# Kernel tuning notes

Hardware: AMD Instinct MI355X
Metric: run time of the kernel (lower is better)

Reference implementation:

```python
import jax, jax.numpy as jnp
import numpy as np

N_NODES = 100000
N_EDGES = 3200000
H, D = 3, 12  # heads, per-head dim; H*D == node_hidden_dim == 36
NEG_SLOPE = 0.2


def setup_inputs() -> dict:
    key = jax.random.key(0)
    ks = jax.random.split(key, 11)
    s = 0.1
    return {
        "node_features": jax.random.normal(ks[0], (N_NODES, 36), jnp.float32),
        "src": jax.random.randint(ks[1], (N_EDGES,), 0, N_NODES),
        "dst": jax.random.randint(ks[2], (N_EDGES,), 0, N_NODES),
        "lin0_w": jax.random.normal(ks[3], (36, 36), jnp.float32) * s,
        "lin0_b": jax.random.normal(ks[4], (36,), jnp.float32) * s,
        "fc_w": jax.random.normal(ks[5], (3, 36, 36), jnp.float32) * s,
        "attn_l": jax.random.normal(ks[6], (3, H, D), jnp.float32) * s,
        "attn_r": jax.random.normal(ks[7], (3, H, D), jnp.float32) * s,
        "gat_bias": jax.random.normal(ks[8], (3, 36), jnp.float32) * s,
        "out_w": jax.random.normal(ks[9], (36, 36), jnp.float32) * s,
        "out_b": jax.random.normal(ks[10], (36,), jnp.float32) * s,
    }


def _gat_layer(h, src, dst, fc_w, a_l, a_r, bias):
    n = h.shape[0]
    feat = (h @ fc_w).reshape(n, H, D)                      # (N,H,D)
    el = jnp.sum(feat * a_l, axis=-1)                       # (N,H)
    er = jnp.sum(feat * a_r, axis=-1)                       # (N,H)
    e = el[src] + er[dst]                                   # (E,H)
    e = jnp.where(e >= 0, e, NEG_SLOPE * e)                 # leaky_relu(0.2)
    # edge softmax over incoming edges of each dst node (numerically stable)
    m = jax.ops.segment_max(e, dst, num_segments=n)         # (N,H)
    m = jnp.where(jnp.isfinite(m), m, 0.0)                  # zero-degree guard
    ee = jnp.exp(e - m[dst])                                # (E,H)
    denom = jax.ops.segment_sum(ee, dst, num_segments=n)    # (N,H)
    alpha = ee / jnp.maximum(denom[dst], 1e-9)              # (E,H)
    msg = feat[src] * alpha[:, :, None]                     # (E,H,D)
    rst = jax.ops.segment_sum(msg, dst, num_segments=n)     # (N,H,D)
    # residual (Identity since in_feats == H*D) + bias, then ELU
    rst = rst + h.reshape(n, H, D) + bias.reshape(1, H, D)
    return jax.nn.elu(rst).reshape(n, H * D)


def reference(node_features, src, dst, lin0_w, lin0_b, fc_w, attn_l, attn_r, gat_bias, out_w, out_b):
    h = node_features @ lin0_w + lin0_b
    for l in range(3):
        h = _gat_layer(h, src, dst, fc_w[l], attn_l[l], attn_r[l], gat_bias[l])
    return h @ out_w + out_b
```

## Files before the change

### kernel.cpp

```cpp
#include <hip/hip_runtime.h>
#include <math.h>

#define HID 36
#define NH 3
#define HD 12
#define PROW 64
#define BSHIFT 13
#define NBUCK 13
#define PSHIFT 8
#define PCHUNK 2048
#define SPCAP 9216
#define CSRCAP 4096
#define NSTEP 8

typedef _Float16 f16;


__global__ void hist2_kernel(const int* __restrict__ dst, int* __restrict__ M,
                             int E, int C, int np) {
    __shared__ int h[512];
    int t = threadIdx.x;
    int c = blockIdx.x;
    for (int i = t; i < 512; i += blockDim.x) h[i] = 0;
    __syncthreads();
    int i0 = c * PCHUNK;
    int i1 = min(i0 + PCHUNK, E);
    for (int i = i0 + t; i < i1; i += blockDim.x)
        atomicAdd(&h[dst[i] >> PSHIFT], 1);
    __syncthreads();
    for (int b = t; b < np; b += blockDim.x)
        M[(size_t)b * C + c] = h[b];
}

__global__ void base_scan_kernel(const int* __restrict__ M, int* __restrict__ BaseT,
                                 int* __restrict__ T, int C, int np) {
    __shared__ int tmp[512];
    int b = blockIdx.x;
    int t = threadIdx.x;
    int carry = 0;
    for (int base = 0; base < C; base += 512) {
        int idx = base + t;
        int v = (idx < C) ? M[(size_t)b * C + idx] : 0;
        tmp[t] = v;
        __syncthreads();
        for (int ofs = 1; ofs < 512; ofs <<= 1) {
            int x = 0;
            if (t >= ofs) x = tmp[t - ofs];
            __syncthreads();
            tmp[t] += x;
            __syncthreads();
        }
        if (idx < C) BaseT[(size_t)idx * 512 + b] = carry + tmp[t] - v;
        carry += tmp[511];
        __syncthreads();
    }
    if (t == 0) T[b] = carry;
}

__global__ void scan_small_kernel(const int* __restrict__ T, int* __restrict__ poff, int np) {
    __shared__ int tmp[512];
    int t = threadIdx.x;
    int v = (t < np) ? T[t] : 0;
    tmp[t] = v;
    __syncthreads();
    for (int ofs = 1; ofs < 512; ofs <<= 1) {
        int x = 0;
        if (t >= ofs) x = tmp[t - ofs];
        __syncthreads();
        tmp[t] += x;
        __syncthreads();
    }
    int excl = tmp[t] - v;
    if (t < np) poff[t] = excl;
    if (t == np - 1) poff[np] = excl + v;
}

__global__ void part_scatter_kernel(const int* __restrict__ src, const int* __restrict__ dst,
                                    const int* __restrict__ BaseT, const int* __restrict__ poff,
                                    int* __restrict__ part, int E, int np) {
    __shared__ int h[512];
    __shared__ int base[512];
    int t = threadIdx.x;
    int c = blockIdx.x;
    for (int i = t; i < 512; i += blockDim.x) h[i] = 0;
    for (int b = t; b < np; b += blockDim.x)
        base[b] = poff[b] + BaseT[(size_t)c * 512 + b];
    __syncthreads();
    int i0 = c * PCHUNK;
    int i1 = min(i0 + PCHUNK, E);
    for (int i = i0 + t; i < i1; i += blockDim.x) {
        int d = dst[i];
        int bin = d >> PSHIFT;
        int r = atomicAdd(&h[bin], 1);
        part[base[bin] + r] = (src[i] << PSHIFT) | (d & ((1 << PSHIFT) - 1));
    }
}

__global__ void bucket_csr_kernel(const int* __restrict__ part, const int* __restrict__ T,
                                  const int* __restrict__ poff,
                                  int* __restrict__ csr, int* __restrict__ off,
                                  int n, int E) {
    __shared__ int cnt[256 * NBUCK];
    __shared__ int psum[512];
    __shared__ int smpart[SPCAP];
    int p = blockIdx.x;
    int t = threadIdx.x;
    int dbase = p << PSHIFT;
    int nd = min(256, n - dbase);
    int nc = nd * NBUCK;
    for (int i = t; i < nc; i += blockDim.x) cnt[i] = 0;
    __syncthreads();
    int cnt_p = T[p];
    int e0 = poff[p];
    const int* pp = part + e0;
    bool fits = (cnt_p <= SPCAP);
    for (int i = t; i < cnt_p; i += blockDim.x) {
        int e = pp[i];
        if (fits) smpart[i] = e;
        atomicAdd(&cnt[(e & 255) * NBUCK + ((e >> PSHIFT) >> BSHIFT)], 1);
    }
    __syncthreads();
    int sum = 0;
    if (t < nd) {
        for (int k = 0; k < NBUCK; ++k) {
            int c = cnt[t * NBUCK + k];
            cnt[t * NBUCK + k] = sum;
            sum += c;
        }
    }
    psum[t] = (t < nd) ? sum : 0;
    __syncthreads();
    for (int ofs = 1; ofs < 512; ofs <<= 1) {
        int x = 0;
        if (t >= ofs) x = psum[t - ofs];
        __syncthreads();
        psum[t] += x;
        __syncthreads();
    }
    int dexcl = (t > 0) ? psum[t - 1] : 0;
    int start = e0 + dexcl;
    if (t < nd) {
        for (int k = 0; k < NBUCK; ++k) cnt[t * NBUCK + k] += start;
        off[dbase + t] = start;
    }
    __syncthreads();
    for (int i = t; i < cnt_p; i += blockDim.x) {
        int e = fits ? smpart[i] : pp[i];
        int s = e >> PSHIFT;
        int idx = (e & 255) * NBUCK + (s >> BSHIFT);
        int pos = atomicAdd(&cnt[idx], 1);
        csr[pos] = s << 6;
    }
    if (p == 0 && t == 0) off[n] = E;
}


__device__ __forceinline__ void edge_accum(uint4 qa, uint4 qb, float ern,
                                           float& denom, float* acc) {
    union { uint4 q[2]; f16 hx[16]; } v;
    v.q[0] = qa;
    v.q[1] = qb;
    float e = (float)v.hx[12] + ern;
    e = (e >= 0.f) ? e : 0.2f * e;
    float w = __expf(e);
    denom += w;
#pragma unroll
    for (int k = 0; k < HD; ++k) acc[k] += w * (float)v.hx[k];
}

template <bool FITS>
__device__ __forceinline__ void sweep_paced(const int* __restrict__ smbuf,
                                            const int* __restrict__ csre,
                                            int j0, int deg, const f16* __restrict__ pb,
                                            float ern, float& denom, float* acc) {
    int j = j0;
#pragma unroll 1
    for (int s2 = 1; s2 <= NSTEP; ++s2) {
        int jend = j0 + ((deg * s2) >> 3);
        int c = jend - j;
        for (; c >= 4; c -= 4, j += 4) {
            int o0 = FITS ? smbuf[j]     : csre[j];
            int o1 = FITS ? smbuf[j + 1] : csre[j + 1];
            int o2 = FITS ? smbuf[j + 2] : csre[j + 2];
            int o3 = FITS ? smbuf[j + 3] : csre[j + 3];
            const uint4* r0 = (const uint4*)(pb + o0);
            const uint4* r1 = (const uint4*)(pb + o1);
            const uint4* r2 = (const uint4*)(pb + o2);
            const uint4* r3 = (const uint4*)(pb + o3);
            uint4 a0 = r0[0], b0 = r0[1];
            uint4 a1 = r1[0], b1 = r1[1];
            uint4 a2 = r2[0], b2 = r2[1];
            uint4 a3 = r3[0], b3 = r3[1];
            edge_accum(a0, b0, ern, denom, acc);
            edge_accum(a1, b1, ern, denom, acc);
            edge_accum(a2, b2, ern, denom, acc);
            edge_accum(a3, b3, ern, denom, acc);
        }
        for (; c > 0; --c, ++j) {
            int o = FITS ? smbuf[j] : csre[j];
            const uint4* r = (const uint4*)(pb + o);
            edge_accum(r[0], r[1], ern, denom, acc);
        }
    }
}

__global__ void __launch_bounds__(256, 1)
lin0tr_kernel(const float* __restrict__ x, const float* __restrict__ w0,
              const float* __restrict__ b0, const float* __restrict__ fcw,
              const float* __restrict__ al, const float* __restrict__ ar,
              float* __restrict__ h, f16* __restrict__ packed,
              float* __restrict__ er, int n) {
    __shared__ float W0[HID * HID];
    __shared__ float W1[HID * HID];
    __shared__ float Bs[HID], ALs[HID], ARs[HID];
    int t = threadIdx.x;
    for (int i = t; i < HID * HID; i += 256) { W0[i] = w0[i]; W1[i] = fcw[i]; }
    if (t < HID) { Bs[t] = b0[t]; ALs[t] = al[t]; ARs[t] = ar[t]; }
    __syncthreads();
    int node = blockIdx.x * 256 + t;
    if (node >= n) return;
    const float4* xp = (const float4*)(x + (size_t)node * HID);
    float h0[HID];
#pragma unroll
    for (int j = 0; j < HID; ++j) h0[j] = Bs[j];
#pragma unroll
    for (int kk = 0; kk < HID / 4; ++kk) {
        float4 xv = xp[kk];
        const float* w = &W0[(4 * kk) * HID];
#pragma unroll
        for (int j = 0; j < HID; ++j)
            h0[j] += xv.x * w[j] + xv.y * w[HID + j] + xv.z * w[2 * HID + j] + xv.w * w[3 * HID + j];
    }
    float* hp = h + (size_t)node * HID;
#pragma unroll
    for (int j = 0; j < HID; ++j) hp[j] = h0[j];
    float feat[HID];
#pragma unroll
    for (int j = 0; j < HID; ++j) feat[j] = 0.f;
#pragma unroll
    for (int k = 0; k < HID; ++k) {
        float hv = h0[k];
        const float* w = &W1[k * HID];
#pragma unroll
        for (int j = 0; j < HID; ++j) feat[j] += hv * w[j];
    }
    union { f16 hx[48]; uint4 q[6]; } u;
#pragma unroll
    for (int hh = 0; hh < NH; ++hh) {
        float sl = 0.f, sr = 0.f;
#pragma unroll
        for (int d = 0; d < HD; ++d) {
            sl += feat[hh * HD + d] * ALs[hh * HD + d];
            sr += feat[hh * HD + d] * ARs[hh * HD + d];
        }
#pragma unroll
        for (int d = 0; d < HD; ++d) u.hx[hh * 16 + d] = (f16)feat[hh * HD + d];
        u.hx[hh * 16 + 12] = (f16)sl;
        u.hx[hh * 16 + 13] = (f16)0.f;
        u.hx[hh * 16 + 14] = (f16)0.f;
        u.hx[hh * 16 + 15] = (f16)0.f;
        er[node * NH + hh] = sr;
    }
    uint4* prow = (uint4*)(packed + (size_t)node * PROW);
#pragma unroll
    for (int q = 0; q < 6; ++q) prow[q] = u.q[q];
}

__global__ void __launch_bounds__(192)
aggtr_kernel(const f16* __restrict__ packed_in, const float* __restrict__ er_in,
             const float* __restrict__ hcur,
             const int* __restrict__ off, const int* __restrict__ csr,
             const float* __restrict__ bias, const float* __restrict__ wnext,
             const float* __restrict__ aln, const float* __restrict__ arn,
             float* __restrict__ hnext, f16* __restrict__ packed_out,
             float* __restrict__ er_out, int n) {
    __shared__ float Wsh[HID * HID];
    __shared__ float ALs[HID], ARs[HID];
    __shared__ int smbuf[CSRCAP];
    int t = threadIdx.x;
    for (int i = t; i < HID * HID; i += 192) Wsh[i] = wnext[i];
    if (t < HID) { ALs[t] = aln[t]; ARs[t] = arn[t]; }
    int ln = t / 3, hh = t - ln * 3;
    int nb0 = blockIdx.x * 64;
    int node = nb0 + ln;
    bool active = (node < n);

    int e0 = off[nb0];
    int e1 = off[min(nb0 + 64, n)];
    int span = e1 - e0;
    bool fits = (span <= CSRCAP);
    if (fits)
        for (int i = t; i < span; i += 192) smbuf[i] = csr[e0 + i];

    int j0 = 0, deg = 0;
    float ern = 0.f;
    if (active) {
        j0 = off[node] - e0;
        deg = off[node + 1] - e0 - j0;
        ern = er_in[node * NH + hh];
    }
    const f16* pb = packed_in + hh * 16;
    const int* csre = csr + e0;
    __syncthreads();

    float denom = 0.f;
    float acc[HD];
#pragma unroll
    for (int k = 0; k < HD; ++k) acc[k] = 0.f;

    if (fits) sweep_paced<true>(smbuf, csre, j0, deg, pb, ern, denom, acc);
    else      sweep_paced<false>(smbuf, csre, j0, deg, pb, ern, denom, acc);
    __syncthreads();

    float* hsh = (float*)smbuf;
    float v[HD];
#pragma unroll
    for (int k = 0; k < HD; ++k) v[k] = 0.f;
    if (active) {
        float inv = 1.f / fmaxf(denom, 1e-9f);
        int base = node * HID + hh * HD;
        const float4* hc = (const float4*)(hcur + base);
        float4 h0 = hc[0], h1 = hc[1], h2 = hc[2];
        float hres[HD] = {h0.x, h0.y, h0.z, h0.w, h1.x, h1.y, h1.z, h1.w, h2.x, h2.y, h2.z, h2.w};
#pragma unroll
        for (int k = 0; k < HD; ++k) {
            float x = acc[k] * inv + hres[k] + bias[hh * HD + k];
            v[k] = (x > 0.f) ? x : expm1f(x);
        }
        float4* hp = (float4*)(hnext + base);
        hp[0] = make_float4(v[0], v[1], v[2], v[3]);
        hp[1] = make_float4(v[4], v[5], v[6], v[7]);
        hp[2] = make_float4(v[8], v[9], v[10], v[11]);
    }
#pragma unroll
    for (int k = 0; k < HD; ++k) hsh[ln * 37 + hh * HD + k] = v[k];
    __syncthreads();

    float feat[HD];
#pragma unroll
    for (int d = 0; d < HD; ++d) feat[d] = 0.f;
    const float* hrow = &hsh[ln * 37];
#pragma unroll 4
    for (int k = 0; k < HID; ++k) {
        float hv = hrow[k];
        const float* w = &Wsh[k * HID + hh * HD];
#pragma unroll
        for (int d = 0; d < HD; ++d) feat[d] += hv * w[d];
    }
    if (!active) return;
    float sl = 0.f, sr = 0.f;
#pragma unroll
    for (int d = 0; d < HD; ++d) {
        sl += feat[d] * ALs[hh * HD + d];
        sr += feat[d] * ARs[hh * HD + d];
    }
    union { f16 hx[16]; uint4 q[2]; } o;
#pragma unroll
    for (int d = 0; d < HD; ++d) o.hx[d] = (f16)feat[d];
    o.hx[12] = (f16)sl;
    o.hx[13] = (f16)0.f; o.hx[14] = (f16)0.f; o.hx[15] = (f16)0.f;
    uint4* prow = (uint4*)(packed_out + (size_t)node * PROW + hh * 16);
    prow[0] = o.q[0];
    prow[1] = o.q[1];
    er_out[node * NH + hh] = sr;
}

__global__ void __launch_bounds__(192)
aggout_kernel(const f16* __restrict__ packed_in, const float* __restrict__ er_in,
              const float* __restrict__ hcur,
              const int* __restrict__ off, const int* __restrict__ csr,
              const float* __restrict__ bias, const float* __restrict__ ow,
              const float* __restrict__ ob, float* __restrict__ out, int n) {
    __shared__ float Wsh[HID * HID];
    __shared__ float OBs[HID];
    __shared__ int smbuf[CSRCAP];
    int t = threadIdx.x;
    for (int i = t; i < HID * HID; i += 192) Wsh[i] = ow[i];
    if (t < HID) OBs[t] = ob[t];
    int ln = t / 3, hh = t - ln * 3;
    int nb0 = blockIdx.x * 64;
    int node = nb0 + ln;
    bool active = (node < n);

    int e0 = off[nb0];
    int e1 = off[min(nb0 + 64, n)];
    int span = e1 - e0;
    bool fits = (span <= CSRCAP);
    if (fits)
        for (int i = t; i < span; i += 192) smbuf[i] = csr[e0 + i];

    int j0 = 0, deg = 0;
    float ern = 0.f;
    if (active) {
        j0 = off[node] - e0;
        deg = off[node + 1] - e0 - j0;
        ern = er_in[node * NH + hh];
    }
    const f16* pb = packed_in + hh * 16;
    const int* csre = csr + e0;
    __syncthreads();

    float denom = 0.f;
    float acc[HD];
#pragma unroll
    for (int k = 0; k < HD; ++k) acc[k] = 0.f;

    if (fits) sweep_paced<true>(smbuf, csre, j0, deg, pb, ern, denom, acc);
    else      sweep_paced<false>(smbuf, csre, j0, deg, pb, ern, denom, acc);
    __syncthreads();

    float* hsh = (float*)smbuf;
    float v[HD];
#pragma unroll
    for (int k = 0; k < HD; ++k) v[k] = 0.f;
    if (active) {
        float inv = 1.f / fmaxf(denom, 1e-9f);
        int base = node * HID + hh * HD;
        const float4* hc = (const float4*)(hcur + base);
        float4 h0 = hc[0], h1 = hc[1], h2 = hc[2];
        float hres[HD] = {h0.x, h0.y, h0.z, h0.w, h1.x, h1.y, h1.z, h1.w, h2.x, h2.y, h2.z, h2.w};
#pragma unroll
        for (int k = 0; k < HD; ++k) {
            float x = acc[k] * inv + hres[k] + bias[hh * HD + k];
            v[k] = (x > 0.f) ? x : expm1f(x);
        }
    }
#pragma unroll
    for (int k = 0; k < HD; ++k) hsh[ln * 37 + hh * HD + k] = v[k];
    __syncthreads();

    float feat[HD];
#pragma unroll
    for (int d = 0; d < HD; ++d) feat[d] = OBs[hh * HD + d];
    const float* hrow = &hsh[ln * 37];
#pragma unroll 4
    for (int k = 0; k < HID; ++k) {
        float hv = hrow[k];
        const float* w = &Wsh[k * HID + hh * HD];
#pragma unroll
        for (int d = 0; d < HD; ++d) feat[d] += hv * w[d];
    }
    if (!active) return;
    float4* op = (float4*)(out + (size_t)node * HID + hh * HD);
    op[0] = make_float4(feat[0], feat[1], feat[2], feat[3]);
    op[1] = make_float4(feat[4], feat[5], feat[6], feat[7]);
    op[2] = make_float4(feat[8], feat[9], feat[10], feat[11]);
}


extern "C" void kernel_launch(void* const* d_in, const int* in_sizes, int n_in,
                              void* d_out, int out_size, void* d_ws, size_t ws_size,
                              hipStream_t stream) {
    const float* xnf = (const float*)d_in[0];
    const int* src = (const int*)d_in[1];
    const int* dst = (const int*)d_in[2];
    const float* l0w = (const float*)d_in[3];
    const float* l0b = (const float*)d_in[4];
    const float* fcw = (const float*)d_in[5];
    const float* al  = (const float*)d_in[6];
    const float* ar  = (const float*)d_in[7];
    const float* gb  = (const float*)d_in[8];
    const float* ow  = (const float*)d_in[9];
    const float* ob  = (const float*)d_in[10];
    float* out = (float*)d_out;
    const int N = in_sizes[0] / HID;
    const int E = in_sizes[1];
    const int NP = (N + (1 << PSHIFT) - 1) >> PSHIFT;
    const int C = (E + PCHUNK - 1) / PCHUNK;

    char* p = (char*)d_ws;
    auto alloc = [&](size_t bytes) {
        char* r = p;
        p += (bytes + 255) & ~(size_t)255;
        return r;
    };
    int* part    = (int*)alloc((size_t)E * 4);
    int* M       = (int*)alloc((size_t)NP * C * 4);
    int* BaseT   = (int*)alloc((size_t)C * 512 * 4);
    int* T       = (int*)alloc((size_t)NP * 4);
    int* poff    = (int*)alloc((size_t)(NP + 1) * 4);
    int* off     = (int*)alloc((size_t)(N + 1) * 4);
    int* csr     = (int*)alloc((size_t)E * 4);
    float* ha    = (float*)alloc((size_t)N * HID * 4);
    float* hb    = (float*)alloc((size_t)N * HID * 4);
    f16* pkA     = (f16*)alloc((size_t)N * PROW * 2);
    f16* pkB     = (f16*)alloc((size_t)N * PROW * 2);
    float* erA   = (float*)alloc((size_t)N * NH * 4);
    float* erB   = (float*)alloc((size_t)N * NH * 4);

    hist2_kernel<<<C, 512, 0, stream>>>(dst, M, E, C, NP);
    base_scan_kernel<<<NP, 512, 0, stream>>>(M, BaseT, T, C, NP);
    scan_small_kernel<<<1, 512, 0, stream>>>(T, poff, NP);
    part_scatter_kernel<<<C, 512, 0, stream>>>(src, dst, BaseT, poff, part, E, NP);
    bucket_csr_kernel<<<NP, 512, 0, stream>>>(part, T, poff, csr, off, N, E);

    int nblk = (N + 255) / 256;
    int fblk = (N + 63) / 64;

    lin0tr_kernel<<<nblk, 256, 0, stream>>>(xnf, l0w, l0b, fcw, al, ar, ha, pkA, erA, N);

    aggtr_kernel<<<fblk, 192, 0, stream>>>(pkA, erA, ha, off, csr, gb,
                                           fcw + (size_t)1 * HID * HID, al + HID, ar + HID,
                                           hb, pkB, erB, N);
    aggtr_kernel<<<fblk, 192, 0, stream>>>(pkB, erB, hb, off, csr, gb + HID,
                                           fcw + (size_t)2 * HID * HID, al + 2 * HID, ar + 2 * HID,
                                           ha, pkA, erA, N);
    aggout_kernel<<<fblk, 192, 0, stream>>>(pkA, erA, ha, off, csr, gb + 2 * HID,
                                            ow, ob, out, N);
}
```

Before: 367.3 us.

## Fuse lin0 with histogram and fold small scan into consumers

```diff
diff --git a/kernel.cpp b/kernel.cpp
--- a/kernel.cpp
+++ b/kernel.cpp
@@ -16,20 +16,82 @@
 typedef _Float16 f16;
 
 
-__global__ void hist2_kernel(const int* __restrict__ dst, int* __restrict__ M,
-                             int E, int C, int np) {
-    __shared__ int h[512];
+__global__ void __launch_bounds__(256, 1)
+lin0_hist_kernel(const float* __restrict__ x, const float* __restrict__ w0,
+                 const float* __restrict__ b0, const float* __restrict__ fcw,
+                 const float* __restrict__ al, const float* __restrict__ ar,
+                 float* __restrict__ h, f16* __restrict__ packed,
+                 float* __restrict__ er, int n, int nb_lin,
+                 const int* __restrict__ dst, int* __restrict__ M, int E, int C,
+                 int np) {
     int t = threadIdx.x;
-    int c = blockIdx.x;
-    for (int i = t; i < 512; i += blockDim.x) h[i] = 0;
-    __syncthreads();
-    int i0 = c * PCHUNK;
-    int i1 = min(i0 + PCHUNK, E);
-    for (int i = i0 + t; i < i1; i += blockDim.x)
-        atomicAdd(&h[dst[i] >> PSHIFT], 1);
-    __syncthreads();
-    for (int b = t; b < np; b += blockDim.x)
-        M[(size_t)b * C + c] = h[b];
+    if ((int)blockIdx.x >= nb_lin) {
+        __shared__ int hcnt[512];
+        int c = blockIdx.x - nb_lin;
+        for (int i = t; i < 512; i += 256) hcnt[i] = 0;
+        __syncthreads();
+        int i0 = c * PCHUNK;
+        int i1 = min(i0 + PCHUNK, E);
+        for (int i = i0 + t; i < i1; i += 256)
+            atomicAdd(&hcnt[dst[i] >> PSHIFT], 1);
+        __syncthreads();
+        for (int b = t; b < np; b += 256)
+            M[(size_t)b * C + c] = hcnt[b];
+        return;
+    }
+    __shared__ float W0[HID * HID];
+    __shared__ float W1[HID * HID];
+    __shared__ float Bs[HID], ALs[HID], ARs[HID];
+    for (int i = t; i < HID * HID; i += 256) { W0[i] = w0[i]; W1[i] = fcw[i]; }
+    if (t < HID) { Bs[t] = b0[t]; ALs[t] = al[t]; ARs[t] = ar[t]; }
+    __syncthreads();
+    int node = blockIdx.x * 256 + t;
+    if (node >= n) return;
+    const float4* xp = (const float4*)(x + (size_t)node * HID);
+    float h0[HID];
+#pragma unroll
+    for (int j = 0; j < HID; ++j) h0[j] = Bs[j];
+#pragma unroll
+    for (int kk = 0; kk < HID / 4; ++kk) {
+        float4 xv = xp[kk];
+        const float* w = &W0[(4 * kk) * HID];
+#pragma unroll
+        for (int j = 0; j < HID; ++j)
+            h0[j] += xv.x * w[j] + xv.y * w[HID + j] + xv.z * w[2 * HID + j] + xv.w * w[3 * HID + j];
+    }
+    float* hp = h + (size_t)node * HID;
+#pragma unroll
+    for (int j = 0; j < HID; ++j) hp[j] = h0[j];
+    float feat[HID];
+#pragma unroll
+    for (int j = 0; j < HID; ++j) feat[j] = 0.f;
+#pragma unroll
+    for (int k = 0; k < HID; ++k) {
+        float hv = h0[k];
+        const float* w = &W1[k * HID];
+#pragma unroll
+        for (int j = 0; j < HID; ++j) feat[j] += hv * w[j];
+    }
+    union { f16 hx[48]; uint4 q[6]; } u;
+#pragma unroll
+    for (int hh = 0; hh < NH; ++hh) {
+        float sl = 0.f, sr = 0.f;
+#pragma unroll
+        for (int d = 0; d < HD; ++d) {
+            sl += feat[hh * HD + d] * ALs[hh * HD + d];
+            sr += feat[hh * HD + d] * ARs[hh * HD + d];
+        }
+#pragma unroll
+        for (int d = 0; d < HD; ++d) u.hx[hh * 16 + d] = (f16)feat[hh * HD + d];
+        u.hx[hh * 16 + 12] = (f16)sl;
+        u.hx[hh * 16 + 13] = (f16)0.f;
+        u.hx[hh * 16 + 14] = (f16)0.f;
+        u.hx[hh * 16 + 15] = (f16)0.f;
+        er[node * NH + hh] = sr;
+    }
+    uint4* prow = (uint4*)(packed + (size_t)node * PROW);
+#pragma unroll
+    for (int q = 0; q < 6; ++q) prow[q] = u.q[q];
 }
 
 __global__ void base_scan_kernel(const int* __restrict__ M, int* __restrict__ BaseT,
@@ -57,34 +119,26 @@
     if (t == 0) T[b] = carry;
 }
 
-__global__ void scan_small_kernel(const int* __restrict__ T, int* __restrict__ poff, int np) {
-    __shared__ int tmp[512];
-    int t = threadIdx.x;
-    int v = (t < np) ? T[t] : 0;
-    tmp[t] = v;
-    __syncthreads();
-    for (int ofs = 1; ofs < 512; ofs <<= 1) {
-        int x = 0;
-        if (t >= ofs) x = tmp[t - ofs];
-        __syncthreads();
-        tmp[t] += x;
-        __syncthreads();
-    }
-    int excl = tmp[t] - v;
-    if (t < np) poff[t] = excl;
-    if (t == np - 1) poff[np] = excl + v;
-}
-
 __global__ void part_scatter_kernel(const int* __restrict__ src, const int* __restrict__ dst,
-                                    const int* __restrict__ BaseT, const int* __restrict__ poff,
+                                    const int* __restrict__ BaseT, const int* __restrict__ T,
                                     int* __restrict__ part, int E, int np) {
     __shared__ int h[512];
+    __shared__ int tsc[512];
     __shared__ int base[512];
     int t = threadIdx.x;
     int c = blockIdx.x;
-    for (int i = t; i < 512; i += blockDim.x) h[i] = 0;
-    for (int b = t; b < np; b += blockDim.x)
-        base[b] = poff[b] + BaseT[(size_t)c * 512 + b];
+    int v = (t < np) ? T[t] : 0;
+    tsc[t] = v;
+    h[t] = 0;
+    __syncthreads();
+    for (int ofs = 1; ofs < 512; ofs <<= 1) {
+        int x = 0;
+        if (t >= ofs) x = tsc[t - ofs];
+        __syncthreads();
+        tsc[t] += x;
+        __syncthreads();
+    }
+    if (t < np) base[t] = (tsc[t] - v) + BaseT[(size_t)c * 512 + t];
     __syncthreads();
     int i0 = c * PCHUNK;
     int i1 = min(i0 + PCHUNK, E);
@@ -97,21 +151,33 @@
 }
 
 __global__ void bucket_csr_kernel(const int* __restrict__ part, const int* __restrict__ T,
-                                  const int* __restrict__ poff,
                                   int* __restrict__ csr, int* __restrict__ off,
-                                  int n, int E) {
+                                  int n, int E, int np) {
     __shared__ int cnt[256 * NBUCK];
     __shared__ int psum[512];
     __shared__ int smpart[SPCAP];
+    __shared__ int e0s;
     int p = blockIdx.x;
     int t = threadIdx.x;
+    int v = (t < np) ? T[t] : 0;
+    psum[t] = v;
+    __syncthreads();
+    for (int ofs = 1; ofs < 512; ofs <<= 1) {
+        int x = 0;
+        if (t >= ofs) x = psum[t - ofs];
+        __syncthreads();
+        psum[t] += x;
+        __syncthreads();
+    }
+    if (t == p) e0s = psum[t] - v;
+    __syncthreads();
+    int e0 = e0s;
     int dbase = p << PSHIFT;
     int nd = min(256, n - dbase);
     int nc = nd * NBUCK;
     for (int i = t; i < nc; i += blockDim.x) cnt[i] = 0;
     __syncthreads();
     int cnt_p = T[p];
-    int e0 = poff[p];
     const int* pp = part + e0;
     bool fits = (cnt_p <= SPCAP);
     for (int i = t; i < cnt_p; i += blockDim.x) {
@@ -204,68 +270,6 @@
     }
 }
 
-__global__ void __launch_bounds__(256, 1)
-lin0tr_kernel(const float* __restrict__ x, const float* __restrict__ w0,
-              const float* __restrict__ b0, const float* __restrict__ fcw,
-              const float* __restrict__ al, const float* __restrict__ ar,
-              float* __restrict__ h, f16* __restrict__ packed,
-              float* __restrict__ er, int n) {
-    __shared__ float W0[HID * HID];
-    __shared__ float W1[HID * HID];
-    __shared__ float Bs[HID], ALs[HID], ARs[HID];
-    int t = threadIdx.x;
-    for (int i = t; i < HID * HID; i += 256) { W0[i] = w0[i]; W1[i] = fcw[i]; }
-    if (t < HID) { Bs[t] = b0[t]; ALs[t] = al[t]; ARs[t] = ar[t]; }
-    __syncthreads();
-    int node = blockIdx.x * 256 + t;
-    if (node >= n) return;
-    const float4* xp = (const float4*)(x + (size_t)node * HID);
-    float h0[HID];
-#pragma unroll
-    for (int j = 0; j < HID; ++j) h0[j] = Bs[j];
-#pragma unroll
-    for (int kk = 0; kk < HID / 4; ++kk) {
-        float4 xv = xp[kk];
-        const float* w = &W0[(4 * kk) * HID];
-#pragma unroll
-        for (int j = 0; j < HID; ++j)
-            h0[j] += xv.x * w[j] + xv.y * w[HID + j] + xv.z * w[2 * HID + j] + xv.w * w[3 * HID + j];
-    }
-    float* hp = h + (size_t)node * HID;
-#pragma unroll
-    for (int j = 0; j < HID; ++j) hp[j] = h0[j];
-    float feat[HID];
-#pragma unroll
-    for (int j = 0; j < HID; ++j) feat[j] = 0.f;
-#pragma unroll
-    for (int k = 0; k < HID; ++k) {
-        float hv = h0[k];
-        const float* w = &W1[k * HID];
-#pragma unroll
-        for (int j = 0; j < HID; ++j) feat[j] += hv * w[j];
-    }
-    union { f16 hx[48]; uint4 q[6]; } u;
-#pragma unroll
-    for (int hh = 0; hh < NH; ++hh) {
-        float sl = 0.f, sr = 0.f;
-#pragma unroll
-        for (int d = 0; d < HD; ++d) {
-            sl += feat[hh * HD + d] * ALs[hh * HD + d];
-            sr += feat[hh * HD + d] * ARs[hh * HD + d];
-        }
-#pragma unroll
-        for (int d = 0; d < HD; ++d) u.hx[hh * 16 + d] = (f16)feat[hh * HD + d];
-        u.hx[hh * 16 + 12] = (f16)sl;
-        u.hx[hh * 16 + 13] = (f16)0.f;
-        u.hx[hh * 16 + 14] = (f16)0.f;
-        u.hx[hh * 16 + 15] = (f16)0.f;
-        er[node * NH + hh] = sr;
-    }
-    uint4* prow = (uint4*)(packed + (size_t)node * PROW);
-#pragma unroll
-    for (int q = 0; q < 6; ++q) prow[q] = u.q[q];
-}
-
 __global__ void __launch_bounds__(192)
 aggtr_kernel(const f16* __restrict__ packed_in, const float* __restrict__ er_in,
              const float* __restrict__ hcur,
@@ -478,7 +482,6 @@
     int* M       = (int*)alloc((size_t)NP * C * 4);
     int* BaseT   = (int*)alloc((size_t)C * 512 * 4);
     int* T       = (int*)alloc((size_t)NP * 4);
-    int* poff    = (int*)alloc((size_t)(NP + 1) * 4);
     int* off     = (int*)alloc((size_t)(N + 1) * 4);
     int* csr     = (int*)alloc((size_t)E * 4);
     float* ha    = (float*)alloc((size_t)N * HID * 4);
@@ -488,16 +491,15 @@
     float* erA   = (float*)alloc((size_t)N * NH * 4);
     float* erB   = (float*)alloc((size_t)N * NH * 4);
 
-    hist2_kernel<<<C, 512, 0, stream>>>(dst, M, E, C, NP);
-    base_scan_kernel<<<NP, 512, 0, stream>>>(M, BaseT, T, C, NP);
-    scan_small_kernel<<<1, 512, 0, stream>>>(T, poff, NP);
-    part_scatter_kernel<<<C, 512, 0, stream>>>(src, dst, BaseT, poff, part, E, NP);
-    bucket_csr_kernel<<<NP, 512, 0, stream>>>(part, T, poff, csr, off, N, E);
-
     int nblk = (N + 255) / 256;
     int fblk = (N + 63) / 64;
 
-    lin0tr_kernel<<<nblk, 256, 0, stream>>>(xnf, l0w, l0b, fcw, al, ar, ha, pkA, erA, N);
+    lin0_hist_kernel<<<nblk + C, 256, 0, stream>>>(xnf, l0w, l0b, fcw, al, ar,
+                                                   ha, pkA, erA, N, nblk,
+                                                   dst, M, E, C, NP);
+    base_scan_kernel<<<NP, 512, 0, stream>>>(M, BaseT, T, C, NP);
+    part_scatter_kernel<<<C, 512, 0, stream>>>(src, dst, BaseT, T, part, E, NP);
+    bucket_csr_kernel<<<NP, 512, 0, stream>>>(part, T, csr, off, N, E, NP);
 
     aggtr_kernel<<<fblk, 192, 0, stream>>>(pkA, erA, ha, off, csr, gb,
                                            fcw + (size_t)1 * HID * HID, al + HID, ar + HID,
```

New measurement: 367.9 us. Within noise of the previous version (+0.2%).
